# Kernel optimization log

Hardware: AMD Instinct MI355X
Metric: run time of the kernel (lower is better)

The kernel has to match this reference:

```python
import jax, jax.numpy as jnp
import numpy as np

H = 16       # num_heads
D = 128      # head_dim
SCALE = 1.0 / np.sqrt(D).astype(np.float32)


def setup_inputs() -> dict:
    key = jax.random.key(0)
    ks = jax.random.split(key, 5)
    B, S, C = 2, 2048, 2048
    x = jax.random.normal(ks[0], (B, S, C), dtype=jnp.float32)
    # nn.Linear stores weight as [out_features, in_features]; scale ~ kaiming-ish
    s = 1.0 / np.sqrt(C)
    wq = jax.random.normal(ks[1], (C, C), dtype=jnp.float32) * s
    wk = jax.random.normal(ks[2], (C, C), dtype=jnp.float32) * s
    wv = jax.random.normal(ks[3], (C, C), dtype=jnp.float32) * s
    wo = jax.random.normal(ks[4], (C, C), dtype=jnp.float32) * s
    return {"x": x, "wq": wq, "wk": wk, "wv": wv, "wo": wo}


def reference(x, wq, wk, wv, wo):
    B, S, C = x.shape
    # projections: nn.Linear(x) = x @ W.T
    q = (x @ wq.T).reshape(B, S, H, D).transpose(0, 2, 1, 3)  # [B,H,S,D]
    k = (x @ wk.T).reshape(B, S, H, D).transpose(0, 2, 1, 3)
    v = (x @ wv.T).reshape(B, S, H, D).transpose(0, 2, 1, 3)
    scores = jnp.einsum('bhqd,bhkd->bhqk', q, k) * SCALE      # [B,H,S,S]
    attn = jax.nn.softmax(scores, axis=-1)
    out = jnp.einsum('bhqk,bhkd->bhqd', attn, v)              # [B,H,S,D]
    out = out.transpose(0, 2, 1, 3).reshape(B, S, H * D)
    return out @ wo.T
```

## Files before the change

### kernel.cpp

```cpp
#include <hip/hip_runtime.h>
#include <hip/hip_bf16.h>
#include <cstdint>
#include <cstddef>

typedef __bf16 bf16_t;
typedef __bf16 bf8_t __attribute__((ext_vector_type(8)));
typedef float f4_t __attribute__((ext_vector_type(4)));
typedef float f8_t __attribute__((ext_vector_type(8)));

#define DEV static __device__ __forceinline__

DEV f4_t mfma16(bf8_t a, bf8_t b, f4_t c) {
    return __builtin_amdgcn_mfma_f32_16x16x32_bf16(a, b, c, 0, 0, 0);
}

DEV bf8_t cvt8(f8_t v) {
    bf8_t r;
#pragma unroll
    for (int i = 0; i < 8; ++i) r[i] = (bf16_t)v[i];
    return r;
}

DEV void load_lds16(const bf16_t* g, bf16_t* l) {
    __builtin_amdgcn_global_load_lds(
        (const __attribute__((address_space(1))) uint32_t*)g,
        (__attribute__((address_space(3))) uint32_t*)l,
        16, 0, 0);
}

__global__ __launch_bounds__(256) void cvt_fused(const float* __restrict__ x,
                                                 const float* __restrict__ wq,
                                                 const float* __restrict__ wk,
                                                 const float* __restrict__ wv,
                                                 bf16_t* __restrict__ xb,
                                                 bf16_t* __restrict__ wqkvb) {
    const int bid = blockIdx.x;
    const float* src;
    bf16_t* dst;
    int base;
    if (bid < 4096) {
        src = x; dst = xb; base = bid;
    } else {
        const int seg = (bid - 4096) >> 11;
        src = (seg == 0) ? wq : (seg == 1) ? wk : wv;
        dst = wqkvb + (size_t)seg * 4194304;
        base = (bid - 4096) & 2047;
    }
    const size_t i = ((size_t)base * 256 + threadIdx.x) * 8;
    const f8_t v = *(const f8_t*)&src[i];
    *(bf8_t*)&dst[i] = cvt8(v);
}

__global__ __launch_bounds__(256) void cvt_bf16(const float* __restrict__ in,
                                                bf16_t* __restrict__ out, int n8) {
    const int i = blockIdx.x * 256 + threadIdx.x;
    if (i < n8) {
        const f8_t v = *(const f8_t*)&in[(size_t)i * 8];
        *(bf8_t*)&out[(size_t)i * 8] = cvt8(v);
    }
}

__global__ __launch_bounds__(512, 2) void gemm_qkv(const bf16_t* __restrict__ A,
                                                   const bf16_t* __restrict__ B,
                                                   bf16_t* __restrict__ Cq,
                                                   bf16_t* __restrict__ Ck,
                                                   bf16_t* __restrict__ Cv) {
    __shared__ bf16_t smem[73728];

    const int tid = threadIdx.x, lane = tid & 63, wave = tid >> 6;
    const int wr = wave >> 2, wc = wave & 3;
    const int q4 = lane >> 4, r16 = lane & 15;
    const int srow = lane >> 2;
    const int scol = ((lane & 3) ^ ((lane >> 3) & 3)) * 8;
    const int rkey = (r16 >> 1) & 3;

    int wg = blockIdx.y * 24 + blockIdx.x;
    wg = (wg & 7) * 96 + (wg >> 3);
    const int bm0 = (wg / 24) * 128;
    const int bn0 = (wg % 24) * 256;

    f4_t acc[4][4] = {};

    auto stageA = [&](int kt, bf16_t* buf) {
#pragma unroll
        for (int kk = 0; kk < 2; ++kk)
            load_lds16(A + (size_t)(bm0 + wave * 16 + srow) * 2048 + kt * 64 + kk * 32 + scol,
                       buf + kk * 4096 + wave * 16 * 32);
    };
    auto stageB = [&](int kt, bf16_t* buf, int rb) {
#pragma unroll
        for (int kk = 0; kk < 2; ++kk)
            load_lds16(B + (size_t)(bn0 + rb + wave * 16 + srow) * 2048 + kt * 64 + kk * 32 + scol,
                       buf + 8192 + kk * 8192 + (rb + wave * 16) * 32);
    };

    {
        stageA(0, smem);
        stageB(0, smem, 0);
        stageB(0, smem, 128);
        stageA(1, smem + 24576);
        stageB(1, smem + 24576, 0);
        stageB(1, smem + 24576, 128);
        asm volatile("s_waitcnt vmcnt(6)" ::: "memory");
        __builtin_amdgcn_s_barrier();
    }

    int cb = 0, sb = 2;
    for (int t = 0; t < 32; ++t) {
        bf16_t* buf  = smem + cb * 24576;
        bf16_t* sbuf = smem + sb * 24576;

        {
            bf8_t af[4], bq[4];
#pragma unroll
            for (int i = 0; i < 4; ++i)
                af[i] = *(const bf8_t*)&buf[(wr * 64 + i * 16 + r16) * 32 + (q4 ^ rkey) * 8];
#pragma unroll
            for (int n = 0; n < 4; ++n)
                bq[n] = *(const bf8_t*)&buf[8192 + (wc * 64 + n * 16 + r16) * 32 +
                                            (q4 ^ rkey) * 8];
            if (t + 2 < 32) {
                stageA(t + 2, sbuf);
                stageB(t + 2, sbuf, 0);
            }
            __builtin_amdgcn_s_barrier();
            asm volatile("s_waitcnt lgkmcnt(0)" ::: "memory");
            __builtin_amdgcn_s_setprio(1);
#pragma unroll
            for (int i = 0; i < 4; ++i)
#pragma unroll
                for (int n = 0; n < 4; ++n)
                    acc[i][n] = mfma16(af[i], bq[n], acc[i][n]);
            __builtin_amdgcn_s_setprio(0);
            __builtin_amdgcn_s_barrier();
        }

        {
            bf8_t af[4], bq[4];
#pragma unroll
            for (int i = 0; i < 4; ++i)
                af[i] = *(const bf8_t*)&buf[4096 + (wr * 64 + i * 16 + r16) * 32 +
                                            (q4 ^ rkey) * 8];
#pragma unroll
            for (int n = 0; n < 4; ++n)
                bq[n] = *(const bf8_t*)&buf[8192 + 8192 + (wc * 64 + n * 16 + r16) * 32 +
                                            (q4 ^ rkey) * 8];
            if (t + 2 < 32)
                stageB(t + 2, sbuf, 128);
            __builtin_amdgcn_s_barrier();
            asm volatile("s_waitcnt lgkmcnt(0)" ::: "memory");
            __builtin_amdgcn_s_setprio(1);
#pragma unroll
            for (int i = 0; i < 4; ++i)
#pragma unroll
                for (int n = 0; n < 4; ++n)
                    acc[i][n] = mfma16(af[i], bq[n], acc[i][n]);
            __builtin_amdgcn_s_setprio(0);
            if (t < 30) {
                asm volatile("s_waitcnt vmcnt(6)" ::: "memory");
            } else {
                asm volatile("s_waitcnt vmcnt(0)" ::: "memory");
            }
            __builtin_amdgcn_s_barrier();
        }

        cb = (cb == 2) ? 0 : cb + 1;
        sb = (sb == 2) ? 0 : sb + 1;
    }

    __syncthreads();

    bf16_t* strip = smem + wave * 4608;
    if (bn0 < 4096) {
        bf16_t* dst = (bn0 < 2048) ? Cq : Ck;
        const int nb = (bn0 & 2047) + wc * 64;
#pragma unroll
        for (int i = 0; i < 4; ++i)
#pragma unroll
            for (int n = 0; n < 4; ++n)
#pragma unroll
                for (int r = 0; r < 4; ++r)
                    strip[(i * 16 + q4 * 4 + r) * 72 + n * 16 + r16] =
                        (bf16_t)acc[i][n][r];
        asm volatile("s_waitcnt lgkmcnt(0)" ::: "memory");
#pragma unroll
        for (int it = 0; it < 8; ++it) {
            const int row = it * 8 + (lane >> 3);
            const int c = (lane & 7) * 8;
            *(bf8_t*)&dst[(size_t)(bm0 + wr * 64 + row) * 2048 + nb + c] =
                *(const bf8_t*)&strip[row * 72 + c];
        }
    } else {
        const int bb = bm0 >> 11;
        const int s0 = (bm0 & 2047) + wr * 64;
#pragma unroll
        for (int i = 0; i < 4; ++i)
#pragma unroll
            for (int n = 0; n < 4; ++n)
#pragma unroll
                for (int r = 0; r < 4; ++r)
                    strip[(n * 16 + r16) * 72 + i * 16 + q4 * 4 + r] =
                        (bf16_t)acc[i][n][r];
        asm volatile("s_waitcnt lgkmcnt(0)" ::: "memory");
#pragma unroll
        for (int it = 0; it < 8; ++it) {
            const int nrow = it * 8 + (lane >> 3);
            const int c = (lane & 7) * 8;
            const int dg = (bn0 - 4096) + wc * 64 + nrow;
            const int h = dg >> 7, d = dg & 127;
            *(bf8_t*)&Cv[(((size_t)(bb * 16 + h) * 128 + d) << 11) + s0 + c] =
                *(const bf8_t*)&strip[nrow * 72 + c];
        }
    }
}

template <int MODE>
__global__ __launch_bounds__(256) void gemm_m97(const bf16_t* __restrict__ A,
                                                const bf16_t* __restrict__ B,
                                                void* __restrict__ C0,
                                                bf16_t* __restrict__ C1,
                                                bf16_t* __restrict__ C2,
                                                int N, int K) {
    constexpr int SMEMN = (MODE == 0) ? 128 * 136 : 8192;
    __shared__ bf16_t smem[SMEMN];
    bf16_t* As = smem;
    bf16_t* Bs = smem + 4096;

    const int tid = threadIdx.x;
    const int lane = tid & 63;
    const int wave = tid >> 6;
    const int bm0 = blockIdx.y * 128;
    const int bn0 = blockIdx.x * 128;
    const int wm = (wave >> 1) * 64;
    const int wn = (wave & 1) * 64;
    const int q4 = lane >> 4;
    const int r16 = lane & 15;

    const int srow = lane >> 2;
    const int scol = (((lane & 3) ^ ((lane >> 3) & 3))) * 8;
    const int rkey = (r16 >> 1) & 3;

    f4_t acc[4][4] = {};

    for (int k0 = 0; k0 < K; k0 += 32) {
        __syncthreads();
        load_lds16(A + (size_t)(bm0 + wave * 16 + srow) * K + k0 + scol, As + wave * 16 * 32);
        load_lds16(A + (size_t)(bm0 + 64 + wave * 16 + srow) * K + k0 + scol,
                   As + (64 + wave * 16) * 32);
        load_lds16(B + (size_t)(bn0 + wave * 16 + srow) * K + k0 + scol, Bs + wave * 16 * 32);
        load_lds16(B + (size_t)(bn0 + 64 + wave * 16 + srow) * K + k0 + scol,
                   Bs + (64 + wave * 16) * 32);
        __syncthreads();

        bf8_t af[4], bfr[4];
#pragma unroll
        for (int i = 0; i < 4; ++i)
            af[i] = *(const bf8_t*)&As[(wm + i * 16 + r16) * 32 + (q4 ^ rkey) * 8];
#pragma unroll
        for (int j = 0; j < 4; ++j)
            bfr[j] = *(const bf8_t*)&Bs[(wn + j * 16 + r16) * 32 + (q4 ^ rkey) * 8];
#pragma unroll
        for (int i = 0; i < 4; ++i)
#pragma unroll
            for (int j = 0; j < 4; ++j)
                acc[i][j] = mfma16(af[i], bfr[j], acc[i][j]);
    }

    if (MODE == 1) {
        float* C = (float*)C0;
#pragma unroll
        for (int i = 0; i < 4; ++i)
#pragma unroll
            for (int j = 0; j < 4; ++j)
#pragma unroll
                for (int r = 0; r < 4; ++r) {
                    const int m = bm0 + wm + i * 16 + q4 * 4 + r;
                    const int n = bn0 + wn + j * 16 + r16;
                    C[(size_t)m * 2048 + n] = acc[i][j][r];
                }
        return;
    }

    __syncthreads();
    if (bn0 < 4096) {
        bf16_t* dst = (bn0 < 2048) ? (bf16_t*)C0 : C1;
        const int nbase = bn0 & 2047;
#pragma unroll
        for (int i = 0; i < 4; ++i)
#pragma unroll
            for (int j = 0; j < 4; ++j)
#pragma unroll
                for (int r = 0; r < 4; ++r)
                    smem[(wm + i * 16 + q4 * 4 + r) * 136 + wn + j * 16 + r16] =
                        (bf16_t)acc[i][j][r];
        __syncthreads();
#pragma unroll
        for (int it = 0; it < 8; ++it) {
            const int idx = it * 256 + tid;
            const int m = idx >> 4;
            const int nc = (idx & 15) * 8;
            *(bf8_t*)&dst[(size_t)(bm0 + m) * 2048 + nbase + nc] =
                *(const bf8_t*)&smem[m * 136 + nc];
        }
    } else {
#pragma unroll
        for (int i = 0; i < 4; ++i)
#pragma unroll
            for (int j = 0; j < 4; ++j)
#pragma unroll
                for (int r = 0; r < 4; ++r)
                    smem[(wn + j * 16 + r16) * 136 + wm + i * 16 + q4 * 4 + r] =
                        (bf16_t)acc[i][j][r];
        __syncthreads();
        const int bb = bm0 >> 11;
        const int s0 = bm0 & 2047;
        const int nh0 = bn0 - 4096;
#pragma unroll
        for (int it = 0; it < 8; ++it) {
            const int idx = it * 256 + tid;
            const int n = idx >> 4;
            const int mc = (idx & 15) * 8;
            const bf8_t v = *(const bf8_t*)&smem[n * 136 + mc];
            const int dg = nh0 + n;
            const int h = dg >> 7, d = dg & 127;
            *(bf8_t*)&C2[(((size_t)(bb * 16 + h) * 128 + d) << 11) + s0 + mc] = v;
        }
    }
}

__global__ __launch_bounds__(256) void flash5(const bf16_t* __restrict__ Q,
                                              const bf16_t* __restrict__ K,
                                              const bf16_t* __restrict__ VT,
                                              bf16_t* __restrict__ O) {
    constexpr int S = 2048, C = 2048;
    constexpr float SCL = 0.08838834764831845f * 1.4426950408889634f;
    __shared__ bf16_t Ks[4 * 64 * 32];
    __shared__ bf16_t Vs[2 * 128 * 32];
    __shared__ bf16_t Ps[4][32 * 72];

    const int tid = threadIdx.x, lane = tid & 63, wave = tid >> 6;
    const int q4 = lane >> 4, r16 = lane & 15;
    const int bh = blockIdx.y, b = bh >> 4, h = bh & 15;
    const int q0 = blockIdx.x * 128 + wave * 32;

    const size_t qrow = (size_t)b * S + q0;
    const bf16_t* Qp0 = Q + (qrow + r16) * C + h * 128;
    const bf16_t* Qp1 = Q + (qrow + 16 + r16) * C + h * 128;
    const bf16_t* Kbase = K + (size_t)b * S * C + h * 128;
    const bf16_t* Vbase = VT + (size_t)bh * 128 * S;
    bf16_t* Pw = &Ps[wave][0];

    const int srow = lane >> 2;
    const int scol = (((lane & 3) ^ ((lane >> 3) & 3))) * 8;
    const int rkey = (r16 >> 1) & 3;

    bf8_t aq0[4], aq1[4];
#pragma unroll
    for (int kk = 0; kk < 4; ++kk) {
        aq0[kk] = *(const bf8_t*)&Qp0[kk * 32 + q4 * 8];
        aq1[kk] = *(const bf8_t*)&Qp1[kk * 32 + q4 * 8];
    }

    bf8_t ones;
#pragma unroll
    for (int i = 0; i < 8; ++i) ones[i] = (bf16_t)1.0f;

    f4_t o0[8] = {}, o1[8] = {};
    f4_t lacc0 = {}, lacc1 = {};

    for (int kv0 = 0; kv0 < S; kv0 += 64) {
        __syncthreads();
#pragma unroll
        for (int r0 = 0; r0 < 64; r0 += 16)
            load_lds16(Kbase + (size_t)(kv0 + r0 + srow) * C + wave * 32 + scol,
                       Ks + wave * 2048 + r0 * 32);
        {
            const int kkp = wave >> 1;
            const int rb = (wave & 1) * 64;
#pragma unroll
            for (int r0 = 0; r0 < 64; r0 += 16)
                load_lds16(Vbase + (size_t)(rb + r0 + srow) * S + kv0 + kkp * 32 + scol,
                           Vs + kkp * 4096 + (rb + r0) * 32);
        }
        __syncthreads();

        f4_t s4a[4] = {}, s4b[4] = {};
#pragma unroll
        for (int kk = 0; kk < 4; ++kk) {
#pragma unroll
            for (int j = 0; j < 4; ++j) {
                const bf8_t bk =
                    *(const bf8_t*)&Ks[kk * 2048 + (j * 16 + r16) * 32 + (q4 ^ rkey) * 8];
                s4a[j] = mfma16(aq0[kk], bk, s4a[j]);
                s4b[j] = mfma16(aq1[kk], bk, s4b[j]);
            }
        }

#pragma unroll
        for (int r = 0; r < 4; ++r)
#pragma unroll
            for (int j = 0; j < 4; ++j) {
                Pw[(q4 * 4 + r) * 72 + j * 16 + r16] = (bf16_t)exp2f(s4a[j][r] * SCL);
                Pw[(16 + q4 * 4 + r) * 72 + j * 16 + r16] = (bf16_t)exp2f(s4b[j][r] * SCL);
            }
        asm volatile("s_waitcnt lgkmcnt(0)" ::: "memory");

        bf8_t ap0[2], ap1[2];
#pragma unroll
        for (int kkp = 0; kkp < 2; ++kkp) {
            ap0[kkp] = *(const bf8_t*)&Pw[r16 * 72 + kkp * 32 + q4 * 8];
            ap1[kkp] = *(const bf8_t*)&Pw[(16 + r16) * 72 + kkp * 32 + q4 * 8];
        }

#pragma unroll
        for (int kkp = 0; kkp < 2; ++kkp) {
            lacc0 = mfma16(ap0[kkp], ones, lacc0);
            lacc1 = mfma16(ap1[kkp], ones, lacc1);
        }

#pragma unroll
        for (int t = 0; t < 8; ++t) {
#pragma unroll
            for (int kkp = 0; kkp < 2; ++kkp) {
                const bf8_t bv =
                    *(const bf8_t*)&Vs[kkp * 4096 + (t * 16 + r16) * 32 + (q4 ^ rkey) * 8];
                o0[t] = mfma16(ap0[kkp], bv, o0[t]);
                o1[t] = mfma16(ap1[kkp], bv, o1[t]);
            }
        }
    }

    f4_t inv0, inv1;
#pragma unroll
    for (int r = 0; r < 4; ++r) {
        inv0[r] = 1.0f / lacc0[r];
        inv1[r] = 1.0f / lacc1[r];
    }
#pragma unroll
    for (int t = 0; t < 8; ++t)
#pragma unroll
        for (int r = 0; r < 4; ++r) {
            O[(qrow + q4 * 4 + r) * C + h * 128 + t * 16 + r16] = (bf16_t)(o0[t][r] * inv0[r]);
            O[(qrow + 16 + q4 * 4 + r) * C + h * 128 + t * 16 + r16] =
                (bf16_t)(o1[t][r] * inv1[r]);
        }
}

extern "C" void kernel_launch(void* const* d_in, const int* in_sizes, int n_in,
                              void* d_out, int out_size, void* d_ws, size_t ws_size,
                              hipStream_t stream) {
    const float* x  = (const float*)d_in[0];
    const float* wq = (const float*)d_in[1];
    const float* wk = (const float*)d_in[2];
    const float* wv = (const float*)d_in[3];
    const float* wo = (const float*)d_in[4];

    bf16_t* ws = (bf16_t*)d_ws;
    bf16_t* xb   = ws;
    bf16_t* Wqkv = ws + 8388608;
    bf16_t* Qb   = ws + 20971520;
    bf16_t* Kb   = ws + 29360128;
    bf16_t* Vt   = ws + 37748736;
    bf16_t* Wob  = xb;
    bf16_t* At   = Wqkv;

    cvt_fused<<<10240, 256, 0, stream>>>(x, wq, wk, wv, xb, Wqkv);

    gemm_qkv<<<dim3(24, 32), 512, 0, stream>>>(xb, Wqkv, Qb, Kb, Vt);

    cvt_bf16<<<2048, 256, 0, stream>>>(wo, Wob, 524288);

    flash5<<<dim3(16, 32), 256, 0, stream>>>(Qb, Kb, Vt, At);

    gemm_m97<1><<<dim3(16, 32), 256, 0, stream>>>(At, Wob, d_out, nullptr, nullptr, 2048, 2048);
}
```

Baseline: 412.3 us.

## Replace output projection GEMM with triple-buffered 128x256 pipelined kernel

```diff
diff --git a/kernel.cpp b/kernel.cpp
--- a/kernel.cpp
+++ b/kernel.cpp
@@ -214,118 +214,122 @@
     }
 }
 
-template <int MODE>
-__global__ __launch_bounds__(256) void gemm_m97(const bf16_t* __restrict__ A,
-                                                const bf16_t* __restrict__ B,
-                                                void* __restrict__ C0,
-                                                bf16_t* __restrict__ C1,
-                                                bf16_t* __restrict__ C2,
-                                                int N, int K) {
-    constexpr int SMEMN = (MODE == 0) ? 128 * 136 : 8192;
-    __shared__ bf16_t smem[SMEMN];
-    bf16_t* As = smem;
-    bf16_t* Bs = smem + 4096;
-
-    const int tid = threadIdx.x;
-    const int lane = tid & 63;
-    const int wave = tid >> 6;
-    const int bm0 = blockIdx.y * 128;
-    const int bn0 = blockIdx.x * 128;
-    const int wm = (wave >> 1) * 64;
-    const int wn = (wave & 1) * 64;
-    const int q4 = lane >> 4;
-    const int r16 = lane & 15;
-
+__global__ __launch_bounds__(512, 2) void gemm_out(const bf16_t* __restrict__ A,
+                                                   const bf16_t* __restrict__ B,
+                                                   float* __restrict__ C) {
+    __shared__ bf16_t smem[73728];
+
+    const int tid = threadIdx.x, lane = tid & 63, wave = tid >> 6;
+    const int wr = wave >> 2, wc = wave & 3;
+    const int q4 = lane >> 4, r16 = lane & 15;
     const int srow = lane >> 2;
-    const int scol = (((lane & 3) ^ ((lane >> 3) & 3))) * 8;
+    const int scol = ((lane & 3) ^ ((lane >> 3) & 3)) * 8;
     const int rkey = (r16 >> 1) & 3;
 
+    int wg = blockIdx.y * 8 + blockIdx.x;
+    wg = (wg & 7) * 32 + (wg >> 3);
+    const int bm0 = (wg / 8) * 128;
+    const int bn0 = (wg % 8) * 256;
+
     f4_t acc[4][4] = {};
 
-    for (int k0 = 0; k0 < K; k0 += 32) {
-        __syncthreads();
-        load_lds16(A + (size_t)(bm0 + wave * 16 + srow) * K + k0 + scol, As + wave * 16 * 32);
-        load_lds16(A + (size_t)(bm0 + 64 + wave * 16 + srow) * K + k0 + scol,
-                   As + (64 + wave * 16) * 32);
-        load_lds16(B + (size_t)(bn0 + wave * 16 + srow) * K + k0 + scol, Bs + wave * 16 * 32);
-        load_lds16(B + (size_t)(bn0 + 64 + wave * 16 + srow) * K + k0 + scol,
-                   Bs + (64 + wave * 16) * 32);
-        __syncthreads();
-
-        bf8_t af[4], bfr[4];
-#pragma unroll
-        for (int i = 0; i < 4; ++i)
-            af[i] = *(const bf8_t*)&As[(wm + i * 16 + r16) * 32 + (q4 ^ rkey) * 8];
-#pragma unroll
-        for (int j = 0; j < 4; ++j)
-            bfr[j] = *(const bf8_t*)&Bs[(wn + j * 16 + r16) * 32 + (q4 ^ rkey) * 8];
-#pragma unroll
-        for (int i = 0; i < 4; ++i)
-#pragma unroll
-            for (int j = 0; j < 4; ++j)
-                acc[i][j] = mfma16(af[i], bfr[j], acc[i][j]);
-    }
-
-    if (MODE == 1) {
-        float* C = (float*)C0;
-#pragma unroll
-        for (int i = 0; i < 4; ++i)
-#pragma unroll
-            for (int j = 0; j < 4; ++j)
-#pragma unroll
-                for (int r = 0; r < 4; ++r) {
-                    const int m = bm0 + wm + i * 16 + q4 * 4 + r;
-                    const int n = bn0 + wn + j * 16 + r16;
-                    C[(size_t)m * 2048 + n] = acc[i][j][r];
-                }
-        return;
-    }
-
-    __syncthreads();
-    if (bn0 < 4096) {
-        bf16_t* dst = (bn0 < 2048) ? (bf16_t*)C0 : C1;
-        const int nbase = bn0 & 2047;
-#pragma unroll
-        for (int i = 0; i < 4; ++i)
-#pragma unroll
-            for (int j = 0; j < 4; ++j)
-#pragma unroll
-                for (int r = 0; r < 4; ++r)
-                    smem[(wm + i * 16 + q4 * 4 + r) * 136 + wn + j * 16 + r16] =
-                        (bf16_t)acc[i][j][r];
-        __syncthreads();
-#pragma unroll
-        for (int it = 0; it < 8; ++it) {
-            const int idx = it * 256 + tid;
-            const int m = idx >> 4;
-            const int nc = (idx & 15) * 8;
-            *(bf8_t*)&dst[(size_t)(bm0 + m) * 2048 + nbase + nc] =
-                *(const bf8_t*)&smem[m * 136 + nc];
-        }
-    } else {
-#pragma unroll
-        for (int i = 0; i < 4; ++i)
-#pragma unroll
-            for (int j = 0; j < 4; ++j)
-#pragma unroll
-                for (int r = 0; r < 4; ++r)
-                    smem[(wn + j * 16 + r16) * 136 + wm + i * 16 + q4 * 4 + r] =
-                        (bf16_t)acc[i][j][r];
-        __syncthreads();
-        const int bb = bm0 >> 11;
-        const int s0 = bm0 & 2047;
-        const int nh0 = bn0 - 4096;
-#pragma unroll
-        for (int it = 0; it < 8; ++it) {
-            const int idx = it * 256 + tid;
-            const int n = idx >> 4;
-            const int mc = (idx & 15) * 8;
-            const bf8_t v = *(const bf8_t*)&smem[n * 136 + mc];
-            const int dg = nh0 + n;
-            const int h = dg >> 7, d = dg & 127;
-            *(bf8_t*)&C2[(((size_t)(bb * 16 + h) * 128 + d) << 11) + s0 + mc] = v;
-        }
-    }
+    auto stageA = [&](int kt, bf16_t* buf) {
+#pragma unroll
+        for (int kk = 0; kk < 2; ++kk)
+            load_lds16(A + (size_t)(bm0 + wave * 16 + srow) * 2048 + kt * 64 + kk * 32 + scol,
+                       buf + kk * 4096 + wave * 16 * 32);
+    };
+    auto stageB = [&](int kt, bf16_t* buf, int rb) {
+#pragma unroll
+        for (int kk = 0; kk < 2; ++kk)
+            load_lds16(B + (size_t)(bn0 + rb + wave * 16 + srow) * 2048 + kt * 64 + kk * 32 + scol,
+                       buf + 8192 + kk * 8192 + (rb + wave * 16) * 32);
+    };
+
+    {
+        stageA(0, smem);
+        stageB(0, smem, 0);
+        stageB(0, smem, 128);
+        stageA(1, smem + 24576);
+        stageB(1, smem + 24576, 0);
+        stageB(1, smem + 24576, 128);
+        asm volatile("s_waitcnt vmcnt(6)" ::: "memory");
+        __builtin_amdgcn_s_barrier();
+    }
+
+    int cb = 0, sb = 2;
+    for (int t = 0; t < 32; ++t) {
+        bf16_t* buf  = smem + cb * 24576;
+        bf16_t* sbuf = smem + sb * 24576;
+
+        {
+            bf8_t af[4], bq[4];
+#pragma unroll
+            for (int i = 0; i < 4; ++i)
+                af[i] = *(const bf8_t*)&buf[(wr * 64 + i * 16 + r16) * 32 + (q4 ^ rkey) * 8];
+#pragma unroll
+            for (int n = 0; n < 4; ++n)
+                bq[n] = *(const bf8_t*)&buf[8192 + (wc * 64 + n * 16 + r16) * 32 +
+                                            (q4 ^ rkey) * 8];
+            if (t + 2 < 32) {
+                stageA(t + 2, sbuf);
+                stageB(t + 2, sbuf, 0);
+            }
+            __builtin_amdgcn_s_barrier();
+            asm volatile("s_waitcnt lgkmcnt(0)" ::: "memory");
+            __builtin_amdgcn_s_setprio(1);
+#pragma unroll
+            for (int i = 0; i < 4; ++i)
+#pragma unroll
+                for (int n = 0; n < 4; ++n)
+                    acc[i][n] = mfma16(af[i], bq[n], acc[i][n]);
+            __builtin_amdgcn_s_setprio(0);
+            __builtin_amdgcn_s_barrier();
+        }
+
+        {
+            bf8_t af[4], bq[4];
+#pragma unroll
+            for (int i = 0; i < 4; ++i)
+                af[i] = *(const bf8_t*)&buf[4096 + (wr * 64 + i * 16 + r16) * 32 +
+                                            (q4 ^ rkey) * 8];
+#pragma unroll
+            for (int n = 0; n < 4; ++n)
+                bq[n] = *(const bf8_t*)&buf[8192 + 8192 + (wc * 64 + n * 16 + r16) * 32 +
+                                            (q4 ^ rkey) * 8];
+            if (t + 2 < 32)
+                stageB(t + 2, sbuf, 128);
+            __builtin_amdgcn_s_barrier();
+            asm volatile("s_waitcnt lgkmcnt(0)" ::: "memory");
+            __builtin_amdgcn_s_setprio(1);
+#pragma unroll
+            for (int i = 0; i < 4; ++i)
+#pragma unroll
+                for (int n = 0; n < 4; ++n)
+                    acc[i][n] = mfma16(af[i], bq[n], acc[i][n]);
+            __builtin_amdgcn_s_setprio(0);
+            if (t < 30) {
+                asm volatile("s_waitcnt vmcnt(6)" ::: "memory");
+            } else {
+                asm volatile("s_waitcnt vmcnt(0)" ::: "memory");
+            }
+            __builtin_amdgcn_s_barrier();
+        }
+
+        cb = (cb == 2) ? 0 : cb + 1;
+        sb = (sb == 2) ? 0 : sb + 1;
+    }
+
+#pragma unroll
+    for (int i = 0; i < 4; ++i)
+#pragma unroll
+        for (int n = 0; n < 4; ++n)
+#pragma unroll
+            for (int r = 0; r < 4; ++r) {
+                const int m = bm0 + wr * 64 + i * 16 + q4 * 4 + r;
+                const int nn = bn0 + wc * 64 + n * 16 + r16;
+                C[(size_t)m * 2048 + nn] = acc[i][n][r];
+            }
 }
 
 __global__ __launch_bounds__(256) void flash5(const bf16_t* __restrict__ Q,
@@ -472,5 +476,5 @@
 
     flash5<<<dim3(16, 32), 256, 0, stream>>>(Qb, Kb, Vt, At);
 
-    gemm_m97<1><<<dim3(16, 32), 256, 0, stream>>>(At, Wob, d_out, nullptr, nullptr, 2048, 2048);
-}
+    gemm_out<<<dim3(8, 32), 512, 0, stream>>>(At, Wob, (float*)d_out);
+}
```

Result: faster. 392.8 us (-4.7%).
